# Performance work log

Measured on AMD Instinct MI355X. Metric: run time of the kernel, lower is better.

Reference implementation:

```python
import jax, jax.numpy as jnp
import numpy as np

B, N, C = 2, 2048, 512
H = 8
HD = C // H


def _xavier(key, shape):
    fan_in, fan_out = shape[-1], shape[-2] if len(shape) > 1 else shape[-1]
    limit = float(np.sqrt(6.0 / (fan_in + fan_out)))
    return jax.random.uniform(key, shape, jnp.float32, -limit, limit)


def setup_inputs() -> dict:
    key = jax.random.key(0)
    ks = jax.random.split(key, 8)
    return {
        "x": jax.random.normal(ks[0], (B, N, C), jnp.float32),
        "pos_embedding": jax.random.normal(ks[1], (B, N, C), jnp.float32),
        "Wqkv": _xavier(ks[2], (3 * C, C)),      # nn.Linear(dim, 3*dim, bias=False)
        "Wpos": _xavier(ks[3], (C, C)),          # pos_proj, bias=False
        "u_bias": _xavier(ks[4], (H, HD)),
        "v_bias": _xavier(ks[5], (H, HD)),
        "Wproj": _xavier(ks[6], (C, C)),
        "bproj": jnp.zeros((C,), jnp.float32),
    }


def _relative_shift(ps):
    # ps: [B, H, N, M]
    b, h, n, m = ps.shape
    ps = jnp.pad(ps, ((0, 0), (0, 0), (0, 0), (1, 0)))  # zero column in front
    ps = ps.reshape(b, h, m + 1, n)[:, :, 1:, :]
    return ps.reshape(b, h, n, m)


def reference(x, pos_embedding, Wqkv, Wpos, u_bias, v_bias, Wproj, bproj):
    b, n, c = x.shape
    scale = HD ** -0.5
    qkv = (x @ Wqkv.T).reshape(b, n, 3, H, HD)
    q = qkv[:, :, 0].transpose(0, 2, 1, 3)  # [B,H,N,HD]
    k = qkv[:, :, 1].transpose(0, 2, 1, 3)
    v = qkv[:, :, 2].transpose(0, 2, 1, 3)
    pos = (pos_embedding @ Wpos.T).reshape(b, -1, H, HD)  # [B,M,H,HD]

    # content score: (q + u_bias) @ k^T -> [B,H,N,N]
    content = jnp.einsum("bhnd,bhmd->bhnm", q + u_bias[None, :, None, :], k)
    # pos score: (q + v_bias) @ pos^T -> [B,H,N,M]
    pos_score = jnp.einsum("bhnd,bmhd->bhnm", q + v_bias[None, :, None, :], pos)
    pos_score = _relative_shift(pos_score)

    attn = jax.nn.softmax((pos_score + content) * scale, axis=-1)
    out = jnp.einsum("bhnm,bhmd->bhnd", attn, v)
    out = out.transpose(0, 2, 1, 3).reshape(b, n, c)
    return out @ Wproj.T + bproj
```

## Files before the change

kernel.cpp:

```cpp
#include <hip/hip_runtime.h>

typedef __attribute__((ext_vector_type(8))) short bf16x8;
typedef __attribute__((ext_vector_type(4))) short bf16x4;
typedef __attribute__((ext_vector_type(4))) float f32x4;

__device__ __forceinline__ float bf2f(unsigned short u) {
  union { unsigned int i; float f; } c; c.i = ((unsigned int)u) << 16; return c.f;
}
__device__ __forceinline__ unsigned short f2bf(float x) {
  union { float f; unsigned int i; } c; c.f = x;
  return (unsigned short)((c.i + 0x7fffu + ((c.i >> 16) & 1u)) >> 16);
}
__device__ __forceinline__ unsigned int pk2(float a, float b) {
  return (unsigned int)f2bf(a) | ((unsigned int)f2bf(b) << 16);
}

__device__ __forceinline__ uint4 ld8f(const float* p) {
  const float4 a = *(const float4*)p;
  const float4 b = *(const float4*)(p + 4);
  uint4 r;
  r.x = (unsigned)f2bf(a.x) | ((unsigned)f2bf(a.y) << 16);
  r.y = (unsigned)f2bf(a.z) | ((unsigned)f2bf(a.w) << 16);
  r.z = (unsigned)f2bf(b.x) | ((unsigned)f2bf(b.y) << 16);
  r.w = (unsigned)f2bf(b.z) | ((unsigned)f2bf(b.w) << 16);
  return r;
}

__device__ __forceinline__ void gload16(const unsigned short* g, short* l) {
  __builtin_amdgcn_global_load_lds((const __attribute__((address_space(1))) void*)g,
                                   (__attribute__((address_space(3))) void*)l, 16, 0, 0);
}

__global__ __launch_bounds__(256) void k_cvt(const float* __restrict__ x,
    const float* __restrict__ pe, const float* __restrict__ wq,
    const float* __restrict__ wp, const float* __restrict__ wj,
    unsigned short* __restrict__ dst) {
  const long long i8 = ((long long)blockIdx.x * 256 + threadIdx.x) * 8;
  const float* src; long long off;
  if (i8 < 2097152)      { src = x;  off = i8; }
  else if (i8 < 4194304) { src = pe; off = i8 - 2097152; }
  else if (i8 < 4980736) { src = wq; off = i8 - 4194304; }
  else if (i8 < 5242880) { src = wp; off = i8 - 4980736; }
  else                   { src = wj; off = i8 - 5242880; }
  *(uint4*)&dst[i8] = ld8f(src + off);
}

__device__ __forceinline__ void gemm128_mainloop(const unsigned short* __restrict__ Arow,
                                                 const unsigned short* __restrict__ Wrow,
                                                 short* Asl, short* Wsl, f32x4 acc[4][4]) {
  const int tid = threadIdx.x, w = tid >> 6, lane = tid & 63, lm = lane & 15, lq = lane >> 4;
  const int wm = w >> 1, wn = w & 1;
  const int lrow = lane >> 3;
  const int gcol = (((lane & 7) ^ lrow) * 8);
#pragma unroll
  for (int mt = 0; mt < 4; ++mt)
#pragma unroll
    for (int nt = 0; nt < 4; ++nt) acc[mt][nt] = (f32x4){0.f, 0.f, 0.f, 0.f};
#pragma unroll 1
  for (int kc = 0; kc < 512; kc += 64) {
    __syncthreads();
#pragma unroll
    for (int ld = 0; ld < 4; ++ld) {
      const int rbase = w * 32 + ld * 8;
      gload16(&Arow[(size_t)(rbase + lrow) * 512 + kc + gcol], &Asl[rbase * 64]);
      gload16(&Wrow[(size_t)(rbase + lrow) * 512 + kc + gcol], &Wsl[rbase * 64]);
    }
    __syncthreads();
#pragma unroll
    for (int kk = 0; kk < 2; ++kk) {
      const int pcs = ((kk * 4 + lq) ^ (lm & 7)) * 8;
      bf16x8 af[4], bfr[4];
#pragma unroll
      for (int mt = 0; mt < 4; ++mt)
        af[mt] = *(const bf16x8*)&Asl[(wm * 64 + mt * 16 + lm) * 64 + pcs];
#pragma unroll
      for (int nt = 0; nt < 4; ++nt)
        bfr[nt] = *(const bf16x8*)&Wsl[(wn * 64 + nt * 16 + lm) * 64 + pcs];
#pragma unroll
      for (int mt = 0; mt < 4; ++mt)
#pragma unroll
        for (int nt = 0; nt < 4; ++nt)
          acc[mt][nt] = __builtin_amdgcn_mfma_f32_16x16x32_bf16(af[mt], bfr[nt], acc[mt][nt], 0, 0, 0);
    }
  }
}

__device__ __forceinline__ void epi_rows(const f32x4 acc[4][4], const float* __restrict__ bias,
                                         short* TT, unsigned short* __restrict__ dst,
                                         int m0, int cc0) {
  const int tid = threadIdx.x, w = tid >> 6, lane = tid & 63, lm = lane & 15, lq = lane >> 4;
  const int wm = w >> 1, wn = w & 1;
  __syncthreads();
#pragma unroll
  for (int mt = 0; mt < 4; ++mt)
#pragma unroll
    for (int nt = 0; nt < 4; ++nt) {
      const int ccl = wn * 64 + nt * 16 + lm;
      const float bb = bias ? bias[(cc0 + ccl) & 511] : 0.f;
#pragma unroll
      for (int r = 0; r < 4; ++r)
        TT[(wm * 64 + mt * 16 + lq * 4 + r) * 130 + ccl] = (short)f2bf(acc[mt][nt][r] + bb);
    }
  __syncthreads();
#pragma unroll
  for (int rr = 0; rr < 8; ++rr) {
    const int ml = rr * 16 + (tid >> 4), ccl = (tid & 15) * 8;
    const uint4 v = *(const uint4*)&TT[ml * 130 + ccl];
    const int m = m0 + ml, b = m >> 11, n = m & 2047;
    const int cc = cc0 + ccl, hh = (cc >> 6) & 7, d = cc & 63;
    *(uint4*)&dst[((size_t)(b * 8 + hh) * 2048 + n) * 64 + d] = v;
  }
}

__device__ __forceinline__ void epi_cols(const f32x4 acc[4][4], short* TT,
                                         unsigned short* __restrict__ vt,
                                         int m0, int cc0) {
  const int tid = threadIdx.x, w = tid >> 6, lane = tid & 63, lm = lane & 15, lq = lane >> 4;
  const int wm = w >> 1, wn = w & 1;
  __syncthreads();
#pragma unroll
  for (int mt = 0; mt < 4; ++mt)
#pragma unroll
    for (int nt = 0; nt < 4; ++nt) {
      const int ccl = wn * 64 + nt * 16 + lm;
#pragma unroll
      for (int r = 0; r < 4; ++r)
        TT[(wm * 64 + mt * 16 + lq * 4 + r) * 130 + ccl] = (short)f2bf(acc[mt][nt][r]);
    }
  __syncthreads();
  const int b = m0 >> 11;
#pragma unroll
  for (int ss = 0; ss < 8; ++ss) {
    const int ccl = ss * 16 + (tid >> 4), mch = (tid & 15) * 8;
    alignas(16) unsigned short tmp[8];
#pragma unroll
    for (int j = 0; j < 8; ++j) tmp[j] = (unsigned short)TT[(mch + j) * 130 + ccl];
    const int cc = cc0 + ccl, hh = (cc >> 6) & 7, d = cc & 63;
    const int n = (m0 & 2047) + mch;
    *(uint4*)&vt[((size_t)(b * 8 + hh) * 64 + d) * 2048 + n] = *(const uint4*)tmp;
  }
}

__global__ __launch_bounds__(256) void k_gemm_qkvpos(const unsigned short* __restrict__ xb,
    const unsigned short* __restrict__ peb, const unsigned short* __restrict__ wqb,
    const unsigned short* __restrict__ wpb, const float* __restrict__ ub,
    const float* __restrict__ vb, unsigned short* __restrict__ qu,
    unsigned short* __restrict__ qv, unsigned short* __restrict__ kg,
    unsigned short* __restrict__ vt, unsigned short* __restrict__ pos) {
  __shared__ short SB[16640];
  f32x4 acc[4][4];
  const int m0 = blockIdx.y * 128, cc0 = blockIdx.x * 128;
  const unsigned short* Arow = (cc0 < 1536 ? xb : peb) + (size_t)m0 * 512;
  const unsigned short* Wrow = (cc0 < 1536) ? (wqb + (size_t)cc0 * 512)
                                            : (wpb + (size_t)(cc0 - 1536) * 512);
  gemm128_mainloop(Arow, Wrow, SB, SB + 8192, acc);
  const int sec = cc0 >> 9;
  if (sec == 0) {
    epi_rows(acc, ub, SB, qu, m0, cc0);
    epi_rows(acc, vb, SB, qv, m0, cc0);
  } else if (sec == 1) {
    epi_rows(acc, nullptr, SB, kg, m0, cc0);
  } else if (sec == 2) {
    epi_cols(acc, SB, vt, m0, cc0);
  } else {
    epi_rows(acc, nullptr, SB, pos, m0, cc0);
  }
}

__global__ __launch_bounds__(512, 4) void k_flash(const unsigned short* __restrict__ qu,
    const unsigned short* __restrict__ qv, const unsigned short* __restrict__ kg,
    const unsigned short* __restrict__ vt, const unsigned short* __restrict__ posg,
    unsigned short* __restrict__ og) {
  __shared__ short SB[23892];
  short* Ks = SB;
  short* Vs = SB + 4608;
  short* Pn = SB + 9216;
  short* T  = SB + 18432;
  float* Ored = (float*)SB;
  const int tid = threadIdx.x, w = tid >> 6, lane = tid & 63, lm = lane & 15, lq = lane >> 4;
  const int wk = w & 3;
  const int h  = w >> 2;
  const int sw = w >> 1;
  const int ph = w & 1;
  const int hw = blockIdx.x + 32 * blockIdx.y;
  const int xcd = hw & 7, idx = hw >> 3;
  const int bh = xcd * 2 + (idx & 1);
  const int i0 = (idx >> 1) * 64;
  const size_t bhs = (size_t)bh;
  const unsigned short* qub = qu + bhs * (2048 * 64);
  const unsigned short* qvb = qv + bhs * (2048 * 64);
  const unsigned short* pob = posg + bhs * (2048 * 64);
  bf16x8 au[2][2];
#pragma unroll
  for (int qt = 0; qt < 2; ++qt) {
    const int qs = h * 2 + qt;
    au[qt][0] = *(const bf16x8*)&qub[(size_t)(i0 + qs * 16 + lm) * 64 + lq * 8];
    au[qt][1] = *(const bf16x8*)&qub[(size_t)(i0 + qs * 16 + lm) * 64 + 32 + lq * 8];
  }
  const bf16x8 av0 = *(const bf16x8*)&qvb[(size_t)(i0 + sw * 16 + lm) * 64 + lq * 8];
  const bf16x8 av1 = *(const bf16x8*)&qvb[(size_t)(i0 + sw * 16 + lm) * 64 + 32 + lq * 8];
  const int rowe = min(i0 + 49 + lm, 2047);
  const bf16x8 ae0 = *(const bf16x8*)&qvb[(size_t)rowe * 64 + lq * 8];
  const bf16x8 ae1 = *(const bf16x8*)&qvb[(size_t)rowe * 64 + 32 + lq * 8];
  float lsum[2] = {0.f, 0.f};
  f32x4 oacc[2][4];
#pragma unroll
  for (int ii = 0; ii < 2; ++ii)
#pragma unroll
    for (int jj = 0; jj < 4; ++jj) oacc[ii][jj] = (f32x4){0.f, 0.f, 0.f, 0.f};
  const int krow = tid >> 3, kc8 = (tid & 7) * 8;
  const int pb0 = 1983 - i0;
  uint4 kr = *(const uint4*)&kg[(bhs * 2048 + krow) * 64 + kc8];
  uint4 vr = *(const uint4*)&vt[(bhs * 64 + krow) * 2048 + kc8];
  uint4 pr[2];
#pragma unroll
  for (int s = 0; s < 2; ++s) {
    int u = tid + s * 512, prow = u >> 3, c8 = (u & 7) * 8;
    int grow = (pb0 + prow + 4096) & 2047;
    pr[s] = *(const uint4*)&pob[(size_t)grow * 64 + c8];
  }
#pragma unroll 1
  for (int jt = 0; jt < 32; ++jt) {
    const int j0 = jt * 64;
    const int pb = pb0 + j0;
    __syncthreads();
    *(uint4*)&Ks[krow * 72 + kc8] = kr;
    *(uint4*)&Vs[krow * 72 + kc8] = vr;
    if (jt == 0) {
#pragma unroll
      for (int s = 0; s < 2; ++s) {
        int u = tid + s * 512, prow = u >> 3, c8 = (u & 7) * 8;
        int slot = (pb + prow) & 127;
        *(uint4*)&Pn[slot * 72 + c8] = pr[s];
      }
    } else {
      const int slot = (pb + 64 + krow) & 127;
      *(uint4*)&Pn[slot * 72 + kc8] = pr[0];
    }
    __syncthreads();
    if (jt < 31) {
      const int jn = j0 + 64;
      kr = *(const uint4*)&kg[(bhs * 2048 + jn + krow) * 64 + kc8];
      vr = *(const uint4*)&vt[(bhs * 64 + krow) * 2048 + jn + kc8];
      const int grow = (pb + 128 + krow + 4096) & 2047;
      pr[0] = *(const uint4*)&pob[(size_t)grow * 64 + kc8];
    }
    const bf16x8 k0 = *(const bf16x8*)&Ks[(wk * 16 + lm) * 72 + lq * 8];
    const bf16x8 k1 = *(const bf16x8*)&Ks[(wk * 16 + lm) * 72 + 32 + lq * 8];
    f32x4 cacc[2];
#pragma unroll
    for (int qt = 0; qt < 2; ++qt) {
      cacc[qt] = __builtin_amdgcn_mfma_f32_16x16x32_bf16(k0, au[qt][0], (f32x4){0.f,0.f,0.f,0.f}, 0, 0, 0);
      cacc[qt] = __builtin_amdgcn_mfma_f32_16x16x32_bf16(k1, au[qt][1], cacc[qt], 0, 0, 0);
    }
    const int sbase = 49 - sw * 16;
    if (ph == 0) {
#pragma unroll
      for (int ct = 0; ct < 3; ++ct) {
        const int slot = (pb + sbase + ct * 16 + lm) & 127;
        const bf16x8 b0 = *(const bf16x8*)&Pn[slot * 72 + lq * 8];
        const bf16x8 b1 = *(const bf16x8*)&Pn[slot * 72 + 32 + lq * 8];
        f32x4 t0 = __builtin_amdgcn_mfma_f32_16x16x32_bf16(b0, av0, (f32x4){0.f,0.f,0.f,0.f}, 0, 0, 0);
        t0 = __builtin_amdgcn_mfma_f32_16x16x32_bf16(b1, av1, t0, 0, 0, 0);
        uint2 pk; pk.x = pk2(t0[0], t0[1]); pk.y = pk2(t0[2], t0[3]);
        *(uint2*)&T[(sw * 16 + lm) * 84 + ct * 16 + lq * 4] = pk;
      }
    } else {
#pragma unroll
      for (int ct = 3; ct < 5; ++ct) {
        const int slot = (pb + sbase + ct * 16 + lm) & 127;
        const bf16x8 b0 = *(const bf16x8*)&Pn[slot * 72 + lq * 8];
        const bf16x8 b1 = *(const bf16x8*)&Pn[slot * 72 + 32 + lq * 8];
        f32x4 t0 = __builtin_amdgcn_mfma_f32_16x16x32_bf16(b0, av0, (f32x4){0.f,0.f,0.f,0.f}, 0, 0, 0);
        t0 = __builtin_amdgcn_mfma_f32_16x16x32_bf16(b1, av1, t0, 0, 0, 0);
        uint2 pk; pk.x = pk2(t0[0], t0[1]); pk.y = pk2(t0[2], t0[3]);
        *(uint2*)&T[(sw * 16 + lm) * 84 + ct * 16 + lq * 4] = pk;
      }
      {
        const int slot = (pb + sw * 16 + lm) & 127;
        const bf16x8 b0 = *(const bf16x8*)&Pn[slot * 72 + lq * 8];
        const bf16x8 b1 = *(const bf16x8*)&Pn[slot * 72 + 32 + lq * 8];
        f32x4 e0 = __builtin_amdgcn_mfma_f32_16x16x32_bf16(b0, ae0, (f32x4){0.f,0.f,0.f,0.f}, 0, 0, 0);
        e0 = __builtin_amdgcn_mfma_f32_16x16x32_bf16(b1, ae1, e0, 0, 0, 0);
        if (lm == 15) {
          uint2 pk; pk.x = pk2(e0[0], e0[1]); pk.y = pk2(e0[2], e0[3]);
          *(uint2*)&T[64 * 84 + sw * 16 + lq * 4] = pk;
        }
      }
    }
    __syncthreads();
    const int diag = i0 - j0;
    const int jl0 = wk * 16 + lq * 4;
    bf16x4 pf[2];
    if (diag >= 64 || diag <= -128) {
      const int du = (diag <= -128) ? 1 : 0;
      const int rm = lm + du;
#pragma unroll
      for (int qt = 0; qt < 2; ++qt) {
        const int rowa = (h * 2 + qt) * 16 + rm;
        const int base = (rowa == 64) ? (64 * 84 + jl0)
                                      : (rowa * 84 + 15 + jl0 - (rm & 15));
#pragma unroll
        for (int r = 0; r < 4; ++r) {
          const float pv = bf2f((unsigned short)T[base + r]);
          const float p = exp2f((cacc[qt][r] + pv) * 0.18033688f);
          lsum[qt] += p;
          pf[qt][r] = (short)f2bf(p);
        }
      }
    } else {
#pragma unroll
      for (int qt = 0; qt < 2; ++qt) {
        const int qs = h * 2 + qt;
#pragma unroll
        for (int r = 0; r < 4; ++r) {
          const int jl = jl0 + r;
          const int d = (j0 - i0) + jl - (qs * 16 + lm);
          float pv;
          if (d == 1) {
            pv = 0.f;
          } else {
            const int rm2 = lm + ((d > 1) ? 1 : 0);
            const int rowa = qs * 16 + rm2;
            const int base = (rowa == 64) ? (64 * 84 + jl)
                                          : (rowa * 84 + 15 + jl - (rm2 & 15));
            pv = bf2f((unsigned short)T[base]);
          }
          const float p = exp2f((cacc[qt][r] + pv) * 0.18033688f);
          lsum[qt] += p;
          pf[qt][r] = (short)f2bf(p);
        }
      }
    }
#pragma unroll
    for (int dt = 0; dt < 4; ++dt) {
      const bf16x4 vf = *(const bf16x4*)&Vs[(dt * 16 + lm) * 72 + wk * 16 + lq * 4];
      oacc[0][dt] = __builtin_amdgcn_mfma_f32_16x16x16bf16_1k(pf[0], vf, oacc[0][dt], 0, 0, 0);
      oacc[1][dt] = __builtin_amdgcn_mfma_f32_16x16x16bf16_1k(pf[1], vf, oacc[1][dt], 0, 0, 0);
    }
  }
#pragma unroll
  for (int qt = 0; qt < 2; ++qt) {
    lsum[qt] += __shfl_xor(lsum[qt], 16, 64);
    lsum[qt] += __shfl_xor(lsum[qt], 32, 64);
  }
  __syncthreads();
  if (wk == 0) {
#pragma unroll
    for (int qt = 0; qt < 2; ++qt) {
      const int qc = (h * 2 + qt) * 16;
#pragma unroll
      for (int dt = 0; dt < 4; ++dt)
        *(f32x4*)&Ored[(dt * 16 + lm) * 68 + qc + lq * 4] = oacc[qt][dt];
      if (lq == 0) Ored[64 * 68 + qc + lm] = lsum[qt];
    }
  }
  __syncthreads();
#pragma unroll 1
  for (int r = 1; r < 4; ++r) {
    if (wk == r) {
#pragma unroll
      for (int qt = 0; qt < 2; ++qt) {
        const int qc = (h * 2 + qt) * 16;
#pragma unroll
        for (int dt = 0; dt < 4; ++dt) {
          f32x4 o = *(const f32x4*)&Ored[(dt * 16 + lm) * 68 + qc + lq * 4];
          o += oacc[qt][dt];
          *(f32x4*)&Ored[(dt * 16 + lm) * 68 + qc + lq * 4] = o;
        }
        if (lq == 0) Ored[64 * 68 + qc + lm] += lsum[qt];
      }
    }
    __syncthreads();
  }
  if (w < 4) {
    const int b = bh >> 3, hh = bh & 7;
    const f32x4 lv = *(const f32x4*)&Ored[64 * 68 + w * 16 + lq * 4];
    f32x4 inv;
#pragma unroll
    for (int r = 0; r < 4; ++r) inv[r] = 1.f / lv[r];
#pragma unroll
    for (int dt = 0; dt < 4; ++dt) {
      const f32x4 o = *(const f32x4*)&Ored[(dt * 16 + lm) * 68 + w * 16 + lq * 4];
#pragma unroll
      for (int r = 0; r < 4; ++r)
        og[((size_t)b * 2048 + i0 + w * 16 + lq * 4 + r) * 512 + hh * 64 + dt * 16 + lm] =
            f2bf(o[r] * inv[r]);
    }
  }
}

__global__ __launch_bounds__(256) void k_gemm_proj(const unsigned short* __restrict__ og,
    const unsigned short* __restrict__ wjb, const float* __restrict__ bproj,
    float* __restrict__ out) {
  __shared__ short Asl[128 * 64], Wsl[128 * 64];
  f32x4 acc[4][4];
  const int m0 = blockIdx.y * 128, cc0 = blockIdx.x * 128;
  gemm128_mainloop(og + (size_t)m0 * 512, wjb + (size_t)cc0 * 512, Asl, Wsl, acc);
  const int tid = threadIdx.x, w = tid >> 6, lane = tid & 63, lm = lane & 15, lq = lane >> 4;
  const int wm = w >> 1, wn = w & 1;
#pragma unroll
  for (int nt = 0; nt < 4; ++nt) {
    const int cc = cc0 + wn * 64 + nt * 16 + lm;
    const float bias = bproj[cc];
#pragma unroll
    for (int mt = 0; mt < 4; ++mt) {
#pragma unroll
      for (int r = 0; r < 4; ++r) {
        const int m = m0 + wm * 64 + mt * 16 + lq * 4 + r;
        out[(size_t)m * 512 + cc] = acc[mt][nt][r] + bias;
      }
    }
  }
}

extern "C" void kernel_launch(void* const* d_in, const int* in_sizes, int n_in,
                              void* d_out, int out_size, void* d_ws, size_t ws_size,
                              hipStream_t stream) {
  const float* x     = (const float*)d_in[0];
  const float* pe    = (const float*)d_in[1];
  const float* wqkv  = (const float*)d_in[2];
  const float* wpos  = (const float*)d_in[3];
  const float* ub    = (const float*)d_in[4];
  const float* vb    = (const float*)d_in[5];
  const float* wproj = (const float*)d_in[6];
  const float* bproj = (const float*)d_in[7];
  float* out = (float*)d_out;
  unsigned short* ws = (unsigned short*)d_ws;

  const size_t SZ = (size_t)2 * 8 * 2048 * 64;
  unsigned short* qu   = ws;
  unsigned short* qv   = qu + SZ;
  unsigned short* kg   = qv + SZ;
  unsigned short* vt   = kg + SZ;
  unsigned short* pos  = vt + SZ;
  unsigned short* og   = pos + SZ;
  unsigned short* cvtb = og + SZ;
  unsigned short* xb   = cvtb;
  unsigned short* peb  = cvtb + 2097152;
  unsigned short* wqb  = cvtb + 4194304;
  unsigned short* wpb  = cvtb + 4980736;
  unsigned short* wjb  = cvtb + 5242880;

  dim3 blk(256);
  hipLaunchKernelGGL(k_cvt,         dim3(2688),   blk, 0, stream, x, pe, wqkv, wpos, wproj, cvtb);
  hipLaunchKernelGGL(k_gemm_qkvpos, dim3(16, 32), blk, 0, stream,
                     xb, peb, wqb, wpb, ub, vb, qu, qv, kg, vt, pos);
  hipLaunchKernelGGL(k_flash,       dim3(32, 16), dim3(512), 0, stream, qu, qv, kg, vt, pos, og);
  hipLaunchKernelGGL(k_gemm_proj,   dim3(4, 32),  blk, 0, stream, og, wjb, bproj, out);
}
```

Measured before the change: 213.8 us.

## Hoist LDS fragment reads into registers and prefetch K/V/pos two tiles ahead

Moves every LDS fragment read of the current K, V and positional tiles to the top of the loop body, ahead of a single barrier. After that barrier the next tile's data is written into shared memory and the global loads for the tile after it are issued, so global prefetch now runs two tiles ahead. This drops one __syncthreads per iteration and gives the global loads more time to land before use. The cost is more live registers (V and positional fragments), which could lower occupancy or cause spills.

```diff
diff --git a/kernel.cpp b/kernel.cpp
--- a/kernel.cpp
+++ b/kernel.cpp
@@ -210,78 +210,87 @@
     for (int jj = 0; jj < 4; ++jj) oacc[ii][jj] = (f32x4){0.f, 0.f, 0.f, 0.f};
   const int krow = tid >> 3, kc8 = (tid & 7) * 8;
   const int pb0 = 1983 - i0;
-  uint4 kr = *(const uint4*)&kg[(bhs * 2048 + krow) * 64 + kc8];
-  uint4 vr = *(const uint4*)&vt[(bhs * 64 + krow) * 2048 + kc8];
-  uint4 pr[2];
-#pragma unroll
-  for (int s = 0; s < 2; ++s) {
-    int u = tid + s * 512, prow = u >> 3, c8 = (u & 7) * 8;
-    int grow = (pb0 + prow + 4096) & 2047;
-    pr[s] = *(const uint4*)&pob[(size_t)grow * 64 + c8];
-  }
+  {
+    uint4 kr = *(const uint4*)&kg[(bhs * 2048 + krow) * 64 + kc8];
+    uint4 vr = *(const uint4*)&vt[(bhs * 64 + krow) * 2048 + kc8];
+    uint4 p0 = *(const uint4*)&pob[(size_t)((pb0 + krow + 4096) & 2047) * 64 + kc8];
+    uint4 p1 = *(const uint4*)&pob[(size_t)((pb0 + 64 + krow + 4096) & 2047) * 64 + kc8];
+    *(uint4*)&Ks[krow * 72 + kc8] = kr;
+    *(uint4*)&Vs[krow * 72 + kc8] = vr;
+    *(uint4*)&Pn[((pb0 + krow) & 127) * 72 + kc8] = p0;
+    *(uint4*)&Pn[((pb0 + 64 + krow) & 127) * 72 + kc8] = p1;
+  }
+  uint4 kr = *(const uint4*)&kg[(bhs * 2048 + 64 + krow) * 64 + kc8];
+  uint4 vr = *(const uint4*)&vt[(bhs * 64 + krow) * 2048 + 64 + kc8];
+  uint4 pr0 = *(const uint4*)&pob[(size_t)((pb0 + 128 + krow + 4096) & 2047) * 64 + kc8];
+  __syncthreads();
 #pragma unroll 1
   for (int jt = 0; jt < 32; ++jt) {
     const int j0 = jt * 64;
     const int pb = pb0 + j0;
-    __syncthreads();
-    *(uint4*)&Ks[krow * 72 + kc8] = kr;
-    *(uint4*)&Vs[krow * 72 + kc8] = vr;
-    if (jt == 0) {
-#pragma unroll
-      for (int s = 0; s < 2; ++s) {
-        int u = tid + s * 512, prow = u >> 3, c8 = (u & 7) * 8;
-        int slot = (pb + prow) & 127;
-        *(uint4*)&Pn[slot * 72 + c8] = pr[s];
+    const bf16x8 k0 = *(const bf16x8*)&Ks[(wk * 16 + lm) * 72 + lq * 8];
+    const bf16x8 k1 = *(const bf16x8*)&Ks[(wk * 16 + lm) * 72 + 32 + lq * 8];
+    bf16x4 vf[4];
+#pragma unroll
+    for (int dt = 0; dt < 4; ++dt)
+      vf[dt] = *(const bf16x4*)&Vs[(dt * 16 + lm) * 72 + wk * 16 + lq * 4];
+    const int sbase = 49 - sw * 16;
+    bf16x8 pnf[3][2];
+    if (ph == 0) {
+#pragma unroll
+      for (int ct = 0; ct < 3; ++ct) {
+        const int slot = (pb + sbase + ct * 16 + lm) & 127;
+        pnf[ct][0] = *(const bf16x8*)&Pn[slot * 72 + lq * 8];
+        pnf[ct][1] = *(const bf16x8*)&Pn[slot * 72 + 32 + lq * 8];
       }
     } else {
-      const int slot = (pb + 64 + krow) & 127;
-      *(uint4*)&Pn[slot * 72 + kc8] = pr[0];
+#pragma unroll
+      for (int ct = 3; ct < 5; ++ct) {
+        const int slot = (pb + sbase + ct * 16 + lm) & 127;
+        pnf[ct - 3][0] = *(const bf16x8*)&Pn[slot * 72 + lq * 8];
+        pnf[ct - 3][1] = *(const bf16x8*)&Pn[slot * 72 + 32 + lq * 8];
+      }
+      const int slot = (pb + sw * 16 + lm) & 127;
+      pnf[2][0] = *(const bf16x8*)&Pn[slot * 72 + lq * 8];
+      pnf[2][1] = *(const bf16x8*)&Pn[slot * 72 + 32 + lq * 8];
     }
     __syncthreads();
     if (jt < 31) {
-      const int jn = j0 + 64;
-      kr = *(const uint4*)&kg[(bhs * 2048 + jn + krow) * 64 + kc8];
-      vr = *(const uint4*)&vt[(bhs * 64 + krow) * 2048 + jn + kc8];
-      const int grow = (pb + 128 + krow + 4096) & 2047;
-      pr[0] = *(const uint4*)&pob[(size_t)grow * 64 + kc8];
-    }
-    const bf16x8 k0 = *(const bf16x8*)&Ks[(wk * 16 + lm) * 72 + lq * 8];
-    const bf16x8 k1 = *(const bf16x8*)&Ks[(wk * 16 + lm) * 72 + 32 + lq * 8];
+      *(uint4*)&Ks[krow * 72 + kc8] = kr;
+      *(uint4*)&Vs[krow * 72 + kc8] = vr;
+      *(uint4*)&Pn[((pb + 128 + krow) & 127) * 72 + kc8] = pr0;
+      if (jt < 30) {
+        const int jn = j0 + 128;
+        kr = *(const uint4*)&kg[(bhs * 2048 + jn + krow) * 64 + kc8];
+        vr = *(const uint4*)&vt[(bhs * 64 + krow) * 2048 + jn + kc8];
+        pr0 = *(const uint4*)&pob[(size_t)((pb + 192 + krow + 4096) & 2047) * 64 + kc8];
+      }
+    }
     f32x4 cacc[2];
 #pragma unroll
     for (int qt = 0; qt < 2; ++qt) {
       cacc[qt] = __builtin_amdgcn_mfma_f32_16x16x32_bf16(k0, au[qt][0], (f32x4){0.f,0.f,0.f,0.f}, 0, 0, 0);
       cacc[qt] = __builtin_amdgcn_mfma_f32_16x16x32_bf16(k1, au[qt][1], cacc[qt], 0, 0, 0);
     }
-    const int sbase = 49 - sw * 16;
     if (ph == 0) {
 #pragma unroll
       for (int ct = 0; ct < 3; ++ct) {
-        const int slot = (pb + sbase + ct * 16 + lm) & 127;
-        const bf16x8 b0 = *(const bf16x8*)&Pn[slot * 72 + lq * 8];
-        const bf16x8 b1 = *(const bf16x8*)&Pn[slot * 72 + 32 + lq * 8];
-        f32x4 t0 = __builtin_amdgcn_mfma_f32_16x16x32_bf16(b0, av0, (f32x4){0.f,0.f,0.f,0.f}, 0, 0, 0);
-        t0 = __builtin_amdgcn_mfma_f32_16x16x32_bf16(b1, av1, t0, 0, 0, 0);
+        f32x4 t0 = __builtin_amdgcn_mfma_f32_16x16x32_bf16(pnf[ct][0], av0, (f32x4){0.f,0.f,0.f,0.f}, 0, 0, 0);
+        t0 = __builtin_amdgcn_mfma_f32_16x16x32_bf16(pnf[ct][1], av1, t0, 0, 0, 0);
         uint2 pk; pk.x = pk2(t0[0], t0[1]); pk.y = pk2(t0[2], t0[3]);
         *(uint2*)&T[(sw * 16 + lm) * 84 + ct * 16 + lq * 4] = pk;
       }
     } else {
 #pragma unroll
       for (int ct = 3; ct < 5; ++ct) {
-        const int slot = (pb + sbase + ct * 16 + lm) & 127;
-        const bf16x8 b0 = *(const bf16x8*)&Pn[slot * 72 + lq * 8];
-        const bf16x8 b1 = *(const bf16x8*)&Pn[slot * 72 + 32 + lq * 8];
-        f32x4 t0 = __builtin_amdgcn_mfma_f32_16x16x32_bf16(b0, av0, (f32x4){0.f,0.f,0.f,0.f}, 0, 0, 0);
-        t0 = __builtin_amdgcn_mfma_f32_16x16x32_bf16(b1, av1, t0, 0, 0, 0);
+        f32x4 t0 = __builtin_amdgcn_mfma_f32_16x16x32_bf16(pnf[ct - 3][0], av0, (f32x4){0.f,0.f,0.f,0.f}, 0, 0, 0);
+        t0 = __builtin_amdgcn_mfma_f32_16x16x32_bf16(pnf[ct - 3][1], av1, t0, 0, 0, 0);
         uint2 pk; pk.x = pk2(t0[0], t0[1]); pk.y = pk2(t0[2], t0[3]);
         *(uint2*)&T[(sw * 16 + lm) * 84 + ct * 16 + lq * 4] = pk;
       }
       {
-        const int slot = (pb + sw * 16 + lm) & 127;
-        const bf16x8 b0 = *(const bf16x8*)&Pn[slot * 72 + lq * 8];
-        const bf16x8 b1 = *(const bf16x8*)&Pn[slot * 72 + 32 + lq * 8];
-        f32x4 e0 = __builtin_amdgcn_mfma_f32_16x16x32_bf16(b0, ae0, (f32x4){0.f,0.f,0.f,0.f}, 0, 0, 0);
-        e0 = __builtin_amdgcn_mfma_f32_16x16x32_bf16(b1, ae1, e0, 0, 0, 0);
+        f32x4 e0 = __builtin_amdgcn_mfma_f32_16x16x32_bf16(pnf[2][0], ae0, (f32x4){0.f,0.f,0.f,0.f}, 0, 0, 0);
+        e0 = __builtin_amdgcn_mfma_f32_16x16x32_bf16(pnf[2][1], ae1, e0, 0, 0, 0);
         if (lm == 15) {
           uint2 pk; pk.x = pk2(e0[0], e0[1]); pk.y = pk2(e0[2], e0[3]);
           *(uint2*)&T[64 * 84 + sw * 16 + lq * 4] = pk;
@@ -334,9 +343,8 @@
     }
 #pragma unroll
     for (int dt = 0; dt < 4; ++dt) {
-      const bf16x4 vf = *(const bf16x4*)&Vs[(dt * 16 + lm) * 72 + wk * 16 + lq * 4];
-      oacc[0][dt] = __builtin_amdgcn_mfma_f32_16x16x16bf16_1k(pf[0], vf, oacc[0][dt], 0, 0, 0);
-      oacc[1][dt] = __builtin_amdgcn_mfma_f32_16x16x16bf16_1k(pf[1], vf, oacc[1][dt], 0, 0, 0);
+      oacc[0][dt] = __builtin_amdgcn_mfma_f32_16x16x16bf16_1k(pf[0], vf[dt], oacc[0][dt], 0, 0, 0);
+      oacc[1][dt] = __builtin_amdgcn_mfma_f32_16x16x16bf16_1k(pf[1], vf[dt], oacc[1][dt], 0, 0, 0);
     }
   }
 #pragma unroll
```

New measurement: 317.6 us. 1.49x slower.

## Double-buffer K/V/pos tiles with direct global-to-LDS loads and XOR swizzle

Applied to the files above, without the earlier changes.

Replaces the register-staged global loads and LDS stores for the K, V and pos tiles with direct global-to-LDS loads (gload16). K and V get double-buffered LDS tiles so the next tile streams in while the current one is consumed, which removes one __syncthreads per iteration. Padded strides of 72 are replaced by a dense 64-wide layout with an XOR swizzle to avoid bank conflicts. One pos row that would otherwise be overwritten is kept in registers. This raises LDS usage, which may lower occupancy, and it relies on correct swizzle indexing and correct async-load ordering.

```diff
diff --git a/kernel.cpp b/kernel.cpp
--- a/kernel.cpp
+++ b/kernel.cpp
@@ -171,11 +171,11 @@
     const unsigned short* __restrict__ qv, const unsigned short* __restrict__ kg,
     const unsigned short* __restrict__ vt, const unsigned short* __restrict__ posg,
     unsigned short* __restrict__ og) {
-  __shared__ short SB[23892];
-  short* Ks = SB;
-  short* Vs = SB + 4608;
-  short* Pn = SB + 9216;
-  short* T  = SB + 18432;
+  __shared__ short SB[30036];
+  short* KsB = SB;
+  short* VsB = SB + 8192;
+  short* Pn  = SB + 16384;
+  short* T   = SB + 24576;
   float* Ored = (float*)SB;
   const int tid = threadIdx.x, w = tid >> 6, lane = tid & 63, lm = lane & 15, lq = lane >> 4;
   const int wk = w & 3;
@@ -190,6 +190,16 @@
   const unsigned short* qub = qu + bhs * (2048 * 64);
   const unsigned short* qvb = qv + bhs * (2048 * 64);
   const unsigned short* pob = posg + bhs * (2048 * 64);
+  const int x7 = lm & 7;
+  const int kc0 = (lq ^ x7) * 8, kc1 = ((lq + 4) ^ x7) * 8;
+  const int xe = (lm + 7) & 7;
+  const int ec0 = (lq ^ xe) * 8, ec1 = ((lq + 4) ^ xe) * 8;
+  const int ve = (((2 * wk + (lq >> 1)) ^ x7) * 8) + (lq & 1) * 4;
+  const int r0c0 = (lq ^ 7) * 8, r0c1 = ((lq + 4) ^ 7) * 8;
+  const int lrow = lane >> 3;
+  const int gcol = ((lane & 7) ^ lrow) * 8;
+  const unsigned short* ksrc = &kg[(bhs * 2048 + 8 * w + lrow) * 64 + gcol];
+  const unsigned short* vsrc = &vt[(bhs * 64 + 8 * w + lrow) * 2048 + gcol];
   bf16x8 au[2][2];
 #pragma unroll
   for (int qt = 0; qt < 2; ++qt) {
@@ -208,45 +218,37 @@
   for (int ii = 0; ii < 2; ++ii)
 #pragma unroll
     for (int jj = 0; jj < 4; ++jj) oacc[ii][jj] = (f32x4){0.f, 0.f, 0.f, 0.f};
-  const int krow = tid >> 3, kc8 = (tid & 7) * 8;
   const int pb0 = 1983 - i0;
-  uint4 kr = *(const uint4*)&kg[(bhs * 2048 + krow) * 64 + kc8];
-  uint4 vr = *(const uint4*)&vt[(bhs * 64 + krow) * 2048 + kc8];
-  uint4 pr[2];
+  gload16(ksrc, &KsB[w * 512]);
+  gload16(vsrc, &VsB[w * 512]);
 #pragma unroll
   for (int s = 0; s < 2; ++s) {
-    int u = tid + s * 512, prow = u >> 3, c8 = (u & 7) * 8;
-    int grow = (pb0 + prow + 4096) & 2047;
-    pr[s] = *(const uint4*)&pob[(size_t)grow * 64 + c8];
+    const int u = 2 * w + s;
+    const int slotb = (pb0 + 1 + 8 * u) & 127;
+    const int grow = (pb0 + 1 + 8 * u + lrow + 4096) & 2047;
+    gload16(&pob[(size_t)grow * 64 + gcol], &Pn[slotb * 64]);
+  }
+  bf16x8 eb0 = {}, eb1 = {};
+  if (w == 1 && lm == 0) {
+    const int g0 = (pb0 + 4096) & 2047;
+    eb0 = *(const bf16x8*)&pob[(size_t)g0 * 64 + lq * 8];
+    eb1 = *(const bf16x8*)&pob[(size_t)g0 * 64 + 32 + lq * 8];
   }
 #pragma unroll 1
   for (int jt = 0; jt < 32; ++jt) {
     const int j0 = jt * 64;
     const int pb = pb0 + j0;
-    __syncthreads();
-    *(uint4*)&Ks[krow * 72 + kc8] = kr;
-    *(uint4*)&Vs[krow * 72 + kc8] = vr;
-    if (jt == 0) {
-#pragma unroll
-      for (int s = 0; s < 2; ++s) {
-        int u = tid + s * 512, prow = u >> 3, c8 = (u & 7) * 8;
-        int slot = (pb + prow) & 127;
-        *(uint4*)&Pn[slot * 72 + c8] = pr[s];
-      }
-    } else {
-      const int slot = (pb + 64 + krow) & 127;
-      *(uint4*)&Pn[slot * 72 + kc8] = pr[0];
-    }
+    const int nb = jt & 1;
+    short* Ks = KsB + nb * 4096;
+    short* Vs = VsB + nb * 4096;
     __syncthreads();
     if (jt < 31) {
       const int jn = j0 + 64;
-      kr = *(const uint4*)&kg[(bhs * 2048 + jn + krow) * 64 + kc8];
-      vr = *(const uint4*)&vt[(bhs * 64 + krow) * 2048 + jn + kc8];
-      const int grow = (pb + 128 + krow + 4096) & 2047;
-      pr[0] = *(const uint4*)&pob[(size_t)grow * 64 + kc8];
-    }
-    const bf16x8 k0 = *(const bf16x8*)&Ks[(wk * 16 + lm) * 72 + lq * 8];
-    const bf16x8 k1 = *(const bf16x8*)&Ks[(wk * 16 + lm) * 72 + 32 + lq * 8];
+      gload16(ksrc + (size_t)jn * 64, &KsB[(nb ^ 1) * 4096 + w * 512]);
+      gload16(vsrc + jn, &VsB[(nb ^ 1) * 4096 + w * 512]);
+    }
+    const bf16x8 k0 = *(const bf16x8*)&Ks[(wk * 16 + lm) * 64 + kc0];
+    const bf16x8 k1 = *(const bf16x8*)&Ks[(wk * 16 + lm) * 64 + kc1];
     f32x4 cacc[2];
 #pragma unroll
     for (int qt = 0; qt < 2; ++qt) {
@@ -258,8 +260,8 @@
 #pragma unroll
       for (int ct = 0; ct < 3; ++ct) {
         const int slot = (pb + sbase + ct * 16 + lm) & 127;
-        const bf16x8 b0 = *(const bf16x8*)&Pn[slot * 72 + lq * 8];
-        const bf16x8 b1 = *(const bf16x8*)&Pn[slot * 72 + 32 + lq * 8];
+        const bf16x8 b0 = *(const bf16x8*)&Pn[slot * 64 + kc0];
+        const bf16x8 b1 = *(const bf16x8*)&Pn[slot * 64 + kc1];
         f32x4 t0 = __builtin_amdgcn_mfma_f32_16x16x32_bf16(b0, av0, (f32x4){0.f,0.f,0.f,0.f}, 0, 0, 0);
         t0 = __builtin_amdgcn_mfma_f32_16x16x32_bf16(b1, av1, t0, 0, 0, 0);
         uint2 pk; pk.x = pk2(t0[0], t0[1]); pk.y = pk2(t0[2], t0[3]);
@@ -269,26 +271,41 @@
 #pragma unroll
       for (int ct = 3; ct < 5; ++ct) {
         const int slot = (pb + sbase + ct * 16 + lm) & 127;
-        const bf16x8 b0 = *(const bf16x8*)&Pn[slot * 72 + lq * 8];
-        const bf16x8 b1 = *(const bf16x8*)&Pn[slot * 72 + 32 + lq * 8];
+        const bf16x8 b0 = *(const bf16x8*)&Pn[slot * 64 + kc0];
+        const bf16x8 b1 = *(const bf16x8*)&Pn[slot * 64 + kc1];
         f32x4 t0 = __builtin_amdgcn_mfma_f32_16x16x32_bf16(b0, av0, (f32x4){0.f,0.f,0.f,0.f}, 0, 0, 0);
         t0 = __builtin_amdgcn_mfma_f32_16x16x32_bf16(b1, av1, t0, 0, 0, 0);
         uint2 pk; pk.x = pk2(t0[0], t0[1]); pk.y = pk2(t0[2], t0[3]);
         *(uint2*)&T[(sw * 16 + lm) * 84 + ct * 16 + lq * 4] = pk;
       }
       {
-        const int slot = (pb + sw * 16 + lm) & 127;
-        const bf16x8 b0 = *(const bf16x8*)&Pn[slot * 72 + lq * 8];
-        const bf16x8 b1 = *(const bf16x8*)&Pn[slot * 72 + 32 + lq * 8];
+        bf16x8 b0, b1;
+        if (sw == 0 && lm == 0) {
+          b0 = eb0; b1 = eb1;
+        } else {
+          const int slot = (pb + sw * 16 + lm) & 127;
+          b0 = *(const bf16x8*)&Pn[slot * 64 + ec0];
+          b1 = *(const bf16x8*)&Pn[slot * 64 + ec1];
+        }
         f32x4 e0 = __builtin_amdgcn_mfma_f32_16x16x32_bf16(b0, ae0, (f32x4){0.f,0.f,0.f,0.f}, 0, 0, 0);
         e0 = __builtin_amdgcn_mfma_f32_16x16x32_bf16(b1, ae1, e0, 0, 0, 0);
         if (lm == 15) {
           uint2 pk; pk.x = pk2(e0[0], e0[1]); pk.y = pk2(e0[2], e0[3]);
           *(uint2*)&T[64 * 84 + sw * 16 + lq * 4] = pk;
         }
+        if (sw == 0 && lm == 0) {
+          const int sl = (pb + 64) & 127;
+          eb0 = *(const bf16x8*)&Pn[sl * 64 + r0c0];
+          eb1 = *(const bf16x8*)&Pn[sl * 64 + r0c1];
+        }
       }
     }
     __syncthreads();
+    if (jt < 31) {
+      const int slotb = (pb + 129 + 8 * w) & 127;
+      const int grow = (pb + 129 + 8 * w + lrow + 4096) & 2047;
+      gload16(&pob[(size_t)grow * 64 + gcol], &Pn[slotb * 64]);
+    }
     const int diag = i0 - j0;
     const int jl0 = wk * 16 + lq * 4;
     bf16x4 pf[2];
@@ -334,7 +351,7 @@
     }
 #pragma unroll
     for (int dt = 0; dt < 4; ++dt) {
-      const bf16x4 vf = *(const bf16x4*)&Vs[(dt * 16 + lm) * 72 + wk * 16 + lq * 4];
+      const bf16x4 vf = *(const bf16x4*)&Vs[(dt * 16 + lm) * 64 + ve];
       oacc[0][dt] = __builtin_amdgcn_mfma_f32_16x16x16bf16_1k(pf[0], vf, oacc[0][dt], 0, 0, 0);
       oacc[1][dt] = __builtin_amdgcn_mfma_f32_16x16x16bf16_1k(pf[1], vf, oacc[1][dt], 0, 0, 0);
     }
```

Result: faster. 199.9 us (-6.5%).
